# Kernel optimization log

Hardware: AMD Instinct MI355X
Metric: run time of the kernel (lower is better)

Reference implementation:

```python
import jax, jax.numpy as jnp
import numpy as np

B, S, ENC_H, DEC_H, ATTN = 64, 2048, 512, 512, 512


def setup_inputs() -> dict:
    key = jax.random.key(0)
    k1, k2, k3, k4, k5 = jax.random.split(key, 5)
    enc_outputs = jax.random.normal(k1, (B, S, ENC_H), dtype=jnp.float32)
    dec_hidden = jax.random.normal(k2, (B, DEC_H), dtype=jnp.float32)
    # nn.Linear(in, out, bias=False): weight shape [out, in]; y = x @ W.T
    s_enc = 1.0 / np.sqrt(ENC_H)
    s_dec = 1.0 / np.sqrt(DEC_H)
    s_v = 1.0 / np.sqrt(ATTN)
    W_enc = jax.random.uniform(k3, (ATTN, ENC_H), minval=-s_enc, maxval=s_enc, dtype=jnp.float32)
    W_dec = jax.random.uniform(k4, (ATTN, DEC_H), minval=-s_dec, maxval=s_dec, dtype=jnp.float32)
    v = jax.random.uniform(k5, (1, ATTN), minval=-s_v, maxval=s_v, dtype=jnp.float32)
    return {"enc_outputs": enc_outputs, "dec_hidden": dec_hidden,
            "W_enc": W_enc, "W_dec": W_dec, "v": v}


def reference(enc_outputs, dec_hidden, W_enc, W_dec, v):
    # enc_proj: [B,S,A], dec_proj: [B,1,A]
    enc_proj = jnp.einsum('bse,ae->bsa', enc_outputs, W_enc)
    dec_proj = jnp.einsum('bd,ad->ba', dec_hidden, W_dec)[:, None, :]
    score = jnp.einsum('bsa,a->bs', jnp.tanh(enc_proj + dec_proj), v[0])  # [B,S]
    attn_weights = jax.nn.softmax(score, axis=1)
    context = jnp.einsum('bs,bse->be', attn_weights, enc_outputs)  # [B,ENC_H]
    return (context, attn_weights)
```

## Files before the change

### kernel.cpp

```cpp
#include <hip/hip_runtime.h>
#include <hip/hip_bf16.h>

#define B_N 64
#define S_N 2048
#define E_N 512
#define A_N 512

typedef __bf16 bf16x8 __attribute__((ext_vector_type(8)));
typedef float  f32x4  __attribute__((ext_vector_type(4)));

__device__ __forceinline__ unsigned int f2bfu(float f) {
  return (unsigned int)__builtin_bit_cast(unsigned short, (__bf16)f);
}

__global__ __launch_bounds__(256) void k_pack(const float* __restrict__ W,
                                              unsigned short* __restrict__ Wp) {
  const int pk = blockIdx.x * 256 + threadIdx.x;
  const int l = pk & 63, k32 = (pk >> 6) & 15, c = pk >> 10;
  const int ln = l & 15, q = l >> 4;
  const int a = c * 16 + ln, k = k32 * 32 + q * 8;
  const float* src = W + (size_t)a * E_N + k;
  const float4 u = *(const float4*)src;
  const float4 w = *(const float4*)(src + 4);
  uint4 o;
  o.x = f2bfu(u.x) | (f2bfu(u.y) << 16);
  o.y = f2bfu(u.z) | (f2bfu(u.w) << 16);
  o.z = f2bfu(w.x) | (f2bfu(w.y) << 16);
  o.w = f2bfu(w.z) | (f2bfu(w.w) << 16);
  *(uint4*)(Wp + (size_t)pk * 8) = o;
}

__global__ __launch_bounds__(256) void k_decproj(const float* __restrict__ dh,
                                                 const float* __restrict__ Wd,
                                                 float* __restrict__ decp) {
  const int b = blockIdx.x, tid = threadIdx.x;
  __shared__ float h[E_N];
  h[tid] = dh[b * E_N + tid];
  h[tid + 256] = dh[b * E_N + 256 + tid];
  __syncthreads();
  for (int a = tid; a < A_N; a += 256) {
    const float* wr = Wd + (size_t)a * E_N;
    float s = 0.f;
    #pragma unroll 8
    for (int e = 0; e < E_N; e += 4) {
      const float4 w4 = *(const float4*)(wr + e);
      s += w4.x * h[e] + w4.y * h[e + 1] + w4.z * h[e + 2] + w4.w * h[e + 3];
    }
    decp[b * A_N + a] = s;
  }
}

#define RED_OFF (2 * 8192)
#define LDS_TOT (2 * 8192 + 8 * 64 * 4)

__device__ __forceinline__ int a_off(int p, int r, int cb) {
  return p * 8192 + r * 128 + (cb ^ ((r & 7) << 4));
}

__global__ __launch_bounds__(512, 2) void k_scores(
    const float* __restrict__ enc, const unsigned short* __restrict__ Wp,
    const float* __restrict__ decp, const float* __restrict__ vvec,
    float* __restrict__ scores) {
  __shared__ __align__(16) unsigned char lds[LDS_TOT];
  const int tid = threadIdx.x;
  const int lane = tid & 63, wv = tid >> 6, q = lane >> 4, ln = lane & 15;
  const int m0 = blockIdx.x * 64;
  const int b  = m0 >> 11;
  const bf16x8* __restrict__ Wp16 = (const bf16x8*)Wp;

  const int srow = tid >> 3, sc8 = (tid & 7) * 8, scb = (tid & 7) * 16;
  const float* Arow = enc + (size_t)m0 * E_N + (size_t)srow * E_N + sc8;

  {
    const float4 u = *(const float4*)Arow;
    const float4 w = *(const float4*)(Arow + 4);
    uint4 o;
    o.x = f2bfu(u.x) | (f2bfu(u.y) << 16);
    o.y = f2bfu(u.z) | (f2bfu(u.w) << 16);
    o.z = f2bfu(w.x) | (f2bfu(w.y) << 16);
    o.w = f2bfu(w.z) | (f2bfu(w.w) << 16);
    *(uint4*)(lds + a_off(0, srow, scb)) = o;
  }

  f32x4 acc[4][4] = {};

  for (int ks = 0; ks < 8; ++ks) {
    __syncthreads();
    const int p = ks & 1;
    float4 u, w;
    if (ks < 7) {
      u = *(const float4*)(Arow + (ks + 1) * 64);
      w = *(const float4*)(Arow + (ks + 1) * 64 + 4);
    }
    bf16x8 bfr[2][4];
    #pragma unroll
    for (int kt = 0; kt < 2; ++kt) {
      #pragma unroll
      for (int nt = 0; nt < 4; ++nt) {
        const int c = wv * 4 + nt;
        bfr[kt][nt] = Wp16[(c * 16 + ks * 2 + kt) * 64 + lane];
      }
    }
    bf16x8 afr[2][4];
    #pragma unroll
    for (int kt = 0; kt < 2; ++kt)
      #pragma unroll
      for (int mt = 0; mt < 4; ++mt)
        afr[kt][mt] = *(const bf16x8*)(lds + a_off(p, mt * 16 + ln, kt * 64 + q * 16));
    #pragma unroll
    for (int kt = 0; kt < 2; ++kt)
      #pragma unroll
      for (int mt = 0; mt < 4; ++mt)
        #pragma unroll
        for (int nt = 0; nt < 4; ++nt)
          acc[mt][nt] = __builtin_amdgcn_mfma_f32_16x16x32_bf16(afr[kt][mt], bfr[kt][nt], acc[mt][nt], 0, 0, 0);
    if (ks < 7) {
      uint4 o;
      o.x = f2bfu(u.x) | (f2bfu(u.y) << 16);
      o.y = f2bfu(u.z) | (f2bfu(u.w) << 16);
      o.z = f2bfu(w.x) | (f2bfu(w.y) << 16);
      o.w = f2bfu(w.z) | (f2bfu(w.w) << 16);
      *(uint4*)(lds + a_off(p ^ 1, srow, scb)) = o;
    }
  }

  float vv[4], dp[4];
  #pragma unroll
  for (int nt = 0; nt < 4; ++nt) {
    const int a = wv * 64 + nt * 16 + ln;
    vv[nt] = vvec[a];
    dp[nt] = decp[b * A_N + a];
  }
  float part[4][4] = {};
  #pragma unroll
  for (int mt = 0; mt < 4; ++mt)
    #pragma unroll
    for (int nt = 0; nt < 4; ++nt)
      #pragma unroll
      for (int r = 0; r < 4; ++r) {
        float x = acc[mt][nt][r] + dp[nt];
        x = fminf(9.f, fmaxf(-9.f, x));
        const float ex = __expf(2.f * x);
        part[mt][r] = fmaf(__fdividef(ex - 1.f, ex + 1.f), vv[nt], part[mt][r]);
      }
  float* red = (float*)(lds + RED_OFF);
  #pragma unroll
  for (int mt = 0; mt < 4; ++mt)
    #pragma unroll
    for (int r = 0; r < 4; ++r) {
      float s = part[mt][r];
      s += __shfl_xor(s, 1);
      s += __shfl_xor(s, 2);
      s += __shfl_xor(s, 4);
      s += __shfl_xor(s, 8);
      if (ln == 0) red[wv * 64 + mt * 16 + q * 4 + r] = s;
    }
  __syncthreads();
  if (tid < 64) {
    float s = 0.f;
    #pragma unroll
    for (int w8 = 0; w8 < 8; ++w8) s += red[w8 * 64 + tid];
    scores[m0 + tid] = s;
  }
}

__global__ __launch_bounds__(256) void k_softmax(const float* __restrict__ scores,
                                                 float* __restrict__ attn) {
  const int b = blockIdx.x, tid = threadIdx.x;
  float l[8];
  float mx = -3.4e38f;
  #pragma unroll
  for (int i = 0; i < 8; ++i) {
    l[i] = scores[b * S_N + i * 256 + tid];
    mx = fmaxf(mx, l[i]);
  }
  #pragma unroll
  for (int m = 1; m < 64; m <<= 1) mx = fmaxf(mx, __shfl_xor(mx, m));
  __shared__ float sred[8];
  if ((tid & 63) == 0) sred[tid >> 6] = mx;
  __syncthreads();
  mx = fmaxf(fmaxf(sred[0], sred[1]), fmaxf(sred[2], sred[3]));
  float se = 0.f;
  #pragma unroll
  for (int i = 0; i < 8; ++i) { l[i] = __expf(l[i] - mx); se += l[i]; }
  #pragma unroll
  for (int m = 1; m < 64; m <<= 1) se += __shfl_xor(se, m);
  if ((tid & 63) == 0) sred[4 + (tid >> 6)] = se;
  __syncthreads();
  se = sred[4] + sred[5] + sred[6] + sred[7];
  const float inv = 1.f / se;
  #pragma unroll
  for (int i = 0; i < 8; ++i) attn[b * S_N + i * 256 + tid] = l[i] * inv;
}

__global__ __launch_bounds__(512) void k_context(const float* __restrict__ enc,
                                                 const float* __restrict__ attn,
                                                 float* __restrict__ ctx) {
  const int blk = blockIdx.x;
  const int b = blk >> 2, eq = blk & 3;
  const int tid = threadIdx.x;
  const int te = tid & 31, sg = tid >> 5;
  const int e0 = eq * 128 + te * 4;
  const float* ep = enc + (size_t)b * S_N * E_N + e0;
  const float* wp = attn + b * S_N;
  f32x4 acc = {0.f, 0.f, 0.f, 0.f};
  const int s0 = sg * 128;
  #pragma unroll 4
  for (int s = s0; s < s0 + 128; ++s) {
    const float w = wp[s];
    const f32x4 ev = *(const f32x4*)(ep + (size_t)s * E_N);
    acc += w * ev;
  }
  __shared__ f32x4 red[16][32];
  red[sg][te] = acc;
  __syncthreads();
  if (sg == 0) {
    f32x4 t = red[0][te];
    #pragma unroll
    for (int g = 1; g < 16; ++g) t += red[g][te];
    *(f32x4*)(ctx + (size_t)b * E_N + e0) = t;
  }
}

extern "C" void kernel_launch(void* const* d_in, const int* in_sizes, int n_in,
                              void* d_out, int out_size, void* d_ws, size_t ws_size,
                              hipStream_t stream) {
  const float* enc = (const float*)d_in[0];
  const float* dh  = (const float*)d_in[1];
  const float* We  = (const float*)d_in[2];
  const float* Wd  = (const float*)d_in[3];
  const float* v   = (const float*)d_in[4];

  float* out_ctx  = (float*)d_out;
  float* out_attn = out_ctx + B_N * E_N;

  float* scores = (float*)d_ws;
  float* decp   = scores + B_N * S_N;
  unsigned short* Wp = (unsigned short*)(decp + B_N * A_N);

  k_pack   <<<128, 256, 0, stream>>>(We, Wp);
  k_decproj<<<B_N, 256, 0, stream>>>(dh, Wd, decp);
  k_scores <<<(B_N * S_N) / 64, 512, 0, stream>>>(enc, Wp, decp, v, scores);
  k_softmax<<<B_N, 256, 0, stream>>>(scores, out_attn);
  k_context<<<B_N * 4, 512, 0, stream>>>(enc, out_attn, out_ctx);
}
```

Measured before the change: 227.2 us.

## Make score kernel persistent over eight row tiles with full-K LDS double buffering

k_scores now has each block process eight consecutive 64-row tiles. Each tile keeps the whole 512-wide K dimension in LDS as bf16, with two 64KB buffers. The next tile's encoder rows are prefetched into registers in two halves while the current tile's MFMAs run, and W fragments are register-double-buffered across k-steps, so the per-k-step barriers go away. This cuts the grid to one block per CU and removes per-block setup, but the roughly 130KB of LDS limits each CU to a single 512-thread block. The larger register set also risks spilling under the (512,2) launch bounds.

```diff
diff --git a/kernel.cpp b/kernel.cpp
--- a/kernel.cpp
+++ b/kernel.cpp
@@ -50,11 +50,13 @@
   }
 }
 
-#define RED_OFF (2 * 8192)
-#define LDS_TOT (2 * 8192 + 8 * 64 * 4)
+#define TPB 8
+#define ABUF 65536
+#define RED_OFF (2 * ABUF)
+#define LDS_TOT (2 * ABUF + 8 * 64 * 4)
 
 __device__ __forceinline__ int a_off(int p, int r, int cb) {
-  return p * 8192 + r * 128 + (cb ^ ((r & 7) << 4));
+  return p * ABUF + r * 1024 + (cb ^ ((r & 7) << 4));
 }
 
 __global__ __launch_bounds__(512, 2) void k_scores(
@@ -64,103 +66,142 @@
   __shared__ __align__(16) unsigned char lds[LDS_TOT];
   const int tid = threadIdx.x;
   const int lane = tid & 63, wv = tid >> 6, q = lane >> 4, ln = lane & 15;
-  const int m0 = blockIdx.x * 64;
-  const int b  = m0 >> 11;
+  const int row0 = blockIdx.x * (TPB * 64);
+  const int b = row0 >> 11;
   const bf16x8* __restrict__ Wp16 = (const bf16x8*)Wp;
 
-  const int srow = tid >> 3, sc8 = (tid & 7) * 8, scb = (tid & 7) * 16;
-  const float* Arow = enc + (size_t)m0 * E_N + (size_t)srow * E_N + sc8;
-
-  {
-    const float4 u = *(const float4*)Arow;
-    const float4 w = *(const float4*)(Arow + 4);
+  const int srow = tid >> 3, c8 = tid & 7;
+  const float* sbase = enc + (size_t)(row0 + srow) * E_N + c8 * 8;
+
+  float vv[4], dp[4];
+  #pragma unroll
+  for (int nt = 0; nt < 4; ++nt) {
+    const int a = wv * 64 + nt * 16 + ln;
+    vv[nt] = vvec[a];
+    dp[nt] = decp[b * A_N + a];
+  }
+
+  #pragma unroll
+  for (int ksi = 0; ksi < 8; ++ksi) {
+    const float4 u = *(const float4*)(sbase + ksi * 64);
+    const float4 w = *(const float4*)(sbase + ksi * 64 + 4);
     uint4 o;
     o.x = f2bfu(u.x) | (f2bfu(u.y) << 16);
     o.y = f2bfu(u.z) | (f2bfu(u.w) << 16);
     o.z = f2bfu(w.x) | (f2bfu(w.y) << 16);
     o.w = f2bfu(w.z) | (f2bfu(w.w) << 16);
-    *(uint4*)(lds + a_off(0, srow, scb)) = o;
-  }
-
-  f32x4 acc[4][4] = {};
-
-  for (int ks = 0; ks < 8; ++ks) {
+    *(uint4*)(lds + a_off(0, srow, ksi * 128 + c8 * 16)) = o;
+  }
+  __syncthreads();
+
+  float* red = (float*)(lds + RED_OFF);
+
+  for (int t = 0; t < TPB; ++t) {
+    const int bp = t & 1;
+    const float* snext = sbase + (size_t)(t + 1) * 64 * E_N;
+    f32x4 acc[4][4] = {};
+
+    bf16x8 bfr[2][2][4];
+    #pragma unroll
+    for (int kt = 0; kt < 2; ++kt)
+      #pragma unroll
+      for (int nt = 0; nt < 4; ++nt)
+        bfr[0][kt][nt] = Wp16[((wv * 4 + nt) * 16 + kt) * 64 + lane];
+
+    float4 su[4], sw[4];
+    if (t < TPB - 1) {
+      #pragma unroll
+      for (int j = 0; j < 4; ++j) {
+        su[j] = *(const float4*)(snext + j * 64);
+        sw[j] = *(const float4*)(snext + j * 64 + 4);
+      }
+    }
+
+    #pragma unroll
+    for (int ks = 0; ks < 8; ++ks) {
+      const int p = ks & 1;
+      if (ks < 7) {
+        #pragma unroll
+        for (int kt = 0; kt < 2; ++kt)
+          #pragma unroll
+          for (int nt = 0; nt < 4; ++nt)
+            bfr[p ^ 1][kt][nt] =
+                Wp16[((wv * 4 + nt) * 16 + (ks + 1) * 2 + kt) * 64 + lane];
+      }
+      #pragma unroll
+      for (int kt = 0; kt < 2; ++kt) {
+        bf16x8 afr[4];
+        #pragma unroll
+        for (int mt = 0; mt < 4; ++mt)
+          afr[mt] = *(const bf16x8*)(
+              lds + a_off(bp, mt * 16 + ln, ks * 128 + kt * 64 + q * 16));
+        #pragma unroll
+        for (int mt = 0; mt < 4; ++mt)
+          #pragma unroll
+          for (int nt = 0; nt < 4; ++nt)
+            acc[mt][nt] = __builtin_amdgcn_mfma_f32_16x16x32_bf16(
+                afr[mt], bfr[p][kt][nt], acc[mt][nt], 0, 0, 0);
+      }
+      if (ks == 3 && t < TPB - 1) {
+        #pragma unroll
+        for (int j = 0; j < 4; ++j) {
+          uint4 o;
+          o.x = f2bfu(su[j].x) | (f2bfu(su[j].y) << 16);
+          o.y = f2bfu(su[j].z) | (f2bfu(su[j].w) << 16);
+          o.z = f2bfu(sw[j].x) | (f2bfu(sw[j].y) << 16);
+          o.w = f2bfu(sw[j].z) | (f2bfu(sw[j].w) << 16);
+          *(uint4*)(lds + a_off(bp ^ 1, srow, j * 128 + c8 * 16)) = o;
+        }
+        #pragma unroll
+        for (int j = 0; j < 4; ++j) {
+          su[j] = *(const float4*)(snext + (j + 4) * 64);
+          sw[j] = *(const float4*)(snext + (j + 4) * 64 + 4);
+        }
+      }
+    }
+    if (t < TPB - 1) {
+      #pragma unroll
+      for (int j = 0; j < 4; ++j) {
+        uint4 o;
+        o.x = f2bfu(su[j].x) | (f2bfu(su[j].y) << 16);
+        o.y = f2bfu(su[j].z) | (f2bfu(su[j].w) << 16);
+        o.z = f2bfu(sw[j].x) | (f2bfu(sw[j].y) << 16);
+        o.w = f2bfu(sw[j].z) | (f2bfu(sw[j].w) << 16);
+        *(uint4*)(lds + a_off(bp ^ 1, srow, (j + 4) * 128 + c8 * 16)) = o;
+      }
+    }
+
+    float part[4][4] = {};
+    #pragma unroll
+    for (int mt = 0; mt < 4; ++mt)
+      #pragma unroll
+      for (int nt = 0; nt < 4; ++nt)
+        #pragma unroll
+        for (int r = 0; r < 4; ++r) {
+          float x = acc[mt][nt][r] + dp[nt];
+          x = fminf(9.f, fmaxf(-9.f, x));
+          const float ex = __expf(2.f * x);
+          part[mt][r] = fmaf(__fdividef(ex - 1.f, ex + 1.f), vv[nt], part[mt][r]);
+        }
+    #pragma unroll
+    for (int mt = 0; mt < 4; ++mt)
+      #pragma unroll
+      for (int r = 0; r < 4; ++r) {
+        float s = part[mt][r];
+        s += __shfl_xor(s, 1);
+        s += __shfl_xor(s, 2);
+        s += __shfl_xor(s, 4);
+        s += __shfl_xor(s, 8);
+        if (ln == 0) red[wv * 64 + mt * 16 + q * 4 + r] = s;
+      }
     __syncthreads();
-    const int p = ks & 1;
-    float4 u, w;
-    if (ks < 7) {
-      u = *(const float4*)(Arow + (ks + 1) * 64);
-      w = *(const float4*)(Arow + (ks + 1) * 64 + 4);
-    }
-    bf16x8 bfr[2][4];
-    #pragma unroll
-    for (int kt = 0; kt < 2; ++kt) {
-      #pragma unroll
-      for (int nt = 0; nt < 4; ++nt) {
-        const int c = wv * 4 + nt;
-        bfr[kt][nt] = Wp16[(c * 16 + ks * 2 + kt) * 64 + lane];
-      }
-    }
-    bf16x8 afr[2][4];
-    #pragma unroll
-    for (int kt = 0; kt < 2; ++kt)
-      #pragma unroll
-      for (int mt = 0; mt < 4; ++mt)
-        afr[kt][mt] = *(const bf16x8*)(lds + a_off(p, mt * 16 + ln, kt * 64 + q * 16));
-    #pragma unroll
-    for (int kt = 0; kt < 2; ++kt)
-      #pragma unroll
-      for (int mt = 0; mt < 4; ++mt)
-        #pragma unroll
-        for (int nt = 0; nt < 4; ++nt)
-          acc[mt][nt] = __builtin_amdgcn_mfma_f32_16x16x32_bf16(afr[kt][mt], bfr[kt][nt], acc[mt][nt], 0, 0, 0);
-    if (ks < 7) {
-      uint4 o;
-      o.x = f2bfu(u.x) | (f2bfu(u.y) << 16);
-      o.y = f2bfu(u.z) | (f2bfu(u.w) << 16);
-      o.z = f2bfu(w.x) | (f2bfu(w.y) << 16);
-      o.w = f2bfu(w.z) | (f2bfu(w.w) << 16);
-      *(uint4*)(lds + a_off(p ^ 1, srow, scb)) = o;
-    }
-  }
-
-  float vv[4], dp[4];
-  #pragma unroll
-  for (int nt = 0; nt < 4; ++nt) {
-    const int a = wv * 64 + nt * 16 + ln;
-    vv[nt] = vvec[a];
-    dp[nt] = decp[b * A_N + a];
-  }
-  float part[4][4] = {};
-  #pragma unroll
-  for (int mt = 0; mt < 4; ++mt)
-    #pragma unroll
-    for (int nt = 0; nt < 4; ++nt)
-      #pragma unroll
-      for (int r = 0; r < 4; ++r) {
-        float x = acc[mt][nt][r] + dp[nt];
-        x = fminf(9.f, fmaxf(-9.f, x));
-        const float ex = __expf(2.f * x);
-        part[mt][r] = fmaf(__fdividef(ex - 1.f, ex + 1.f), vv[nt], part[mt][r]);
-      }
-  float* red = (float*)(lds + RED_OFF);
-  #pragma unroll
-  for (int mt = 0; mt < 4; ++mt)
-    #pragma unroll
-    for (int r = 0; r < 4; ++r) {
-      float s = part[mt][r];
-      s += __shfl_xor(s, 1);
-      s += __shfl_xor(s, 2);
-      s += __shfl_xor(s, 4);
-      s += __shfl_xor(s, 8);
-      if (ln == 0) red[wv * 64 + mt * 16 + q * 4 + r] = s;
-    }
-  __syncthreads();
-  if (tid < 64) {
-    float s = 0.f;
-    #pragma unroll
-    for (int w8 = 0; w8 < 8; ++w8) s += red[w8 * 64 + tid];
-    scores[m0 + tid] = s;
+    if (tid < 64) {
+      float s = 0.f;
+      #pragma unroll
+      for (int w8 = 0; w8 < 8; ++w8) s += red[w8 * 64 + tid];
+      scores[row0 + t * 64 + tid] = s;
+    }
+    __syncthreads();
   }
 }
 
@@ -240,7 +281,7 @@
 
   k_pack   <<<128, 256, 0, stream>>>(We, Wp);
   k_decproj<<<B_N, 256, 0, stream>>>(dh, Wd, decp);
-  k_scores <<<(B_N * S_N) / 64, 512, 0, stream>>>(enc, Wp, decp, v, scores);
+  k_scores <<<(B_N * S_N) / (TPB * 64), 512, 0, stream>>>(enc, Wp, decp, v, scores);
   k_softmax<<<B_N, 256, 0, stream>>>(scores, out_attn);
   k_context<<<B_N * 4, 512, 0, stream>>>(enc, out_attn, out_ctx);
 }
```

New measurement: 326.8 us. +43.8%, slower.

## Load full A tile into LDS upfront and drop per-step double buffering

Applied to the files above, without the earlier changes.

The scores kernel now converts and stores the whole 64x512 encoder tile into LDS as bf16 before any MFMA work, with each wave loading entire rows for contiguous global reads. The K loop then runs with no barriers between steps. This removes the per-step syncthreads and the interleaved prefetch. In exchange it gives up intra-block overlap of global loads with compute and raises LDS use to about 66 KB per block, which may limit occupancy.

```diff
diff --git a/kernel.cpp b/kernel.cpp
--- a/kernel.cpp
+++ b/kernel.cpp
@@ -50,11 +50,12 @@
   }
 }
 
-#define RED_OFF (2 * 8192)
-#define LDS_TOT (2 * 8192 + 8 * 64 * 4)
-
-__device__ __forceinline__ int a_off(int p, int r, int cb) {
-  return p * 8192 + r * 128 + (cb ^ ((r & 7) << 4));
+#define LDS_A   65536
+#define RED_OFF LDS_A
+#define LDS_TOT (LDS_A + 8 * 64 * 4)
+
+__device__ __forceinline__ int a_off(int r, int kb) {
+  return r * 1024 + (kb ^ ((r & 7) << 4));
 }
 
 __global__ __launch_bounds__(512, 2) void k_scores(
@@ -64,65 +65,9 @@
   __shared__ __align__(16) unsigned char lds[LDS_TOT];
   const int tid = threadIdx.x;
   const int lane = tid & 63, wv = tid >> 6, q = lane >> 4, ln = lane & 15;
-  const int m0 = blockIdx.x * 64;
-  const int b  = m0 >> 11;
+  const int row0 = blockIdx.x * 64;
+  const int b = row0 >> 11;
   const bf16x8* __restrict__ Wp16 = (const bf16x8*)Wp;
-
-  const int srow = tid >> 3, sc8 = (tid & 7) * 8, scb = (tid & 7) * 16;
-  const float* Arow = enc + (size_t)m0 * E_N + (size_t)srow * E_N + sc8;
-
-  {
-    const float4 u = *(const float4*)Arow;
-    const float4 w = *(const float4*)(Arow + 4);
-    uint4 o;
-    o.x = f2bfu(u.x) | (f2bfu(u.y) << 16);
-    o.y = f2bfu(u.z) | (f2bfu(u.w) << 16);
-    o.z = f2bfu(w.x) | (f2bfu(w.y) << 16);
-    o.w = f2bfu(w.z) | (f2bfu(w.w) << 16);
-    *(uint4*)(lds + a_off(0, srow, scb)) = o;
-  }
-
-  f32x4 acc[4][4] = {};
-
-  for (int ks = 0; ks < 8; ++ks) {
-    __syncthreads();
-    const int p = ks & 1;
-    float4 u, w;
-    if (ks < 7) {
-      u = *(const float4*)(Arow + (ks + 1) * 64);
-      w = *(const float4*)(Arow + (ks + 1) * 64 + 4);
-    }
-    bf16x8 bfr[2][4];
-    #pragma unroll
-    for (int kt = 0; kt < 2; ++kt) {
-      #pragma unroll
-      for (int nt = 0; nt < 4; ++nt) {
-        const int c = wv * 4 + nt;
-        bfr[kt][nt] = Wp16[(c * 16 + ks * 2 + kt) * 64 + lane];
-      }
-    }
-    bf16x8 afr[2][4];
-    #pragma unroll
-    for (int kt = 0; kt < 2; ++kt)
-      #pragma unroll
-      for (int mt = 0; mt < 4; ++mt)
-        afr[kt][mt] = *(const bf16x8*)(lds + a_off(p, mt * 16 + ln, kt * 64 + q * 16));
-    #pragma unroll
-    for (int kt = 0; kt < 2; ++kt)
-      #pragma unroll
-      for (int mt = 0; mt < 4; ++mt)
-        #pragma unroll
-        for (int nt = 0; nt < 4; ++nt)
-          acc[mt][nt] = __builtin_amdgcn_mfma_f32_16x16x32_bf16(afr[kt][mt], bfr[kt][nt], acc[mt][nt], 0, 0, 0);
-    if (ks < 7) {
-      uint4 o;
-      o.x = f2bfu(u.x) | (f2bfu(u.y) << 16);
-      o.y = f2bfu(u.z) | (f2bfu(u.w) << 16);
-      o.z = f2bfu(w.x) | (f2bfu(w.y) << 16);
-      o.w = f2bfu(w.z) | (f2bfu(w.w) << 16);
-      *(uint4*)(lds + a_off(p ^ 1, srow, scb)) = o;
-    }
-  }
 
   float vv[4], dp[4];
   #pragma unroll
@@ -131,6 +76,52 @@
     vv[nt] = vvec[a];
     dp[nt] = decp[b * A_N + a];
   }
+
+  {
+    const float* srow = enc + (size_t)(row0 + wv * 8) * E_N + lane * 8;
+    #pragma unroll
+    for (int h = 0; h < 2; ++h) {
+      float4 u[4], w4[4];
+      #pragma unroll
+      for (int j = 0; j < 4; ++j) {
+        u[j]  = *(const float4*)(srow + (size_t)(h * 4 + j) * E_N);
+        w4[j] = *(const float4*)(srow + (size_t)(h * 4 + j) * E_N + 4);
+      }
+      #pragma unroll
+      for (int j = 0; j < 4; ++j) {
+        uint4 o;
+        o.x = f2bfu(u[j].x)  | (f2bfu(u[j].y)  << 16);
+        o.y = f2bfu(u[j].z)  | (f2bfu(u[j].w)  << 16);
+        o.z = f2bfu(w4[j].x) | (f2bfu(w4[j].y) << 16);
+        o.w = f2bfu(w4[j].z) | (f2bfu(w4[j].w) << 16);
+        *(uint4*)(lds + a_off(wv * 8 + h * 4 + j, lane * 16)) = o;
+      }
+    }
+  }
+  __syncthreads();
+
+  f32x4 acc[4][4] = {};
+  #pragma unroll
+  for (int ks = 0; ks < 8; ++ks) {
+    #pragma unroll
+    for (int kt = 0; kt < 2; ++kt) {
+      bf16x8 bfr[4], afr[4];
+      #pragma unroll
+      for (int nt = 0; nt < 4; ++nt)
+        bfr[nt] = Wp16[((wv * 4 + nt) * 16 + ks * 2 + kt) * 64 + lane];
+      #pragma unroll
+      for (int mt = 0; mt < 4; ++mt)
+        afr[mt] = *(const bf16x8*)(
+            lds + a_off(mt * 16 + ln, ks * 128 + kt * 64 + q * 16));
+      #pragma unroll
+      for (int mt = 0; mt < 4; ++mt)
+        #pragma unroll
+        for (int nt = 0; nt < 4; ++nt)
+          acc[mt][nt] = __builtin_amdgcn_mfma_f32_16x16x32_bf16(
+              afr[mt], bfr[nt], acc[mt][nt], 0, 0, 0);
+    }
+  }
+
   float part[4][4] = {};
   #pragma unroll
   for (int mt = 0; mt < 4; ++mt)
@@ -160,7 +151,7 @@
     float s = 0.f;
     #pragma unroll
     for (int w8 = 0; w8 < 8; ++w8) s += red[w8 * 64 + tid];
-    scores[m0 + tid] = s;
+    scores[row0 + tid] = s;
   }
 }
 
```

Measured after the change: 225.8 us. Within noise of the previous version (-0.6%).
